# Kernel tuning notes

Hardware: AMD Instinct MI355X
Metric: run time of the kernel (lower is better)

Reference implementation:

```python
import jax, jax.numpy as jnp
import numpy as np
from jax import lax

BITS = 8

def dec2bin(q, bits=BITS):
    # q: integer-valued float tensor (NCHW or OIHW); stack two's-complement bit-planes along axis 1
    u = jnp.mod(jnp.round(q).astype(jnp.int32), 2 ** bits)
    return jnp.concatenate([((u >> k) & 1) for k in range(bits)], axis=1).astype(jnp.float32)

def quant_sym(x, bits=BITS):
    # brevitas-style signed symmetric per-tensor fake-quant (zero_point = 0)
    n = 2.0 ** (bits - 1) - 1.0
    scale = jnp.max(jnp.abs(x)) / n
    q = jnp.clip(jnp.round(x / scale), -n, n)  # q == value/scale + zero_point
    return q * scale, q

def quant_relu(x, bits=BITS):
    # QuantReLU: unsigned per-tensor fake-quant after relu
    r = jnp.maximum(x, 0.0)
    n = 2.0 ** bits - 1.0
    scale = jnp.max(r) / n
    q = jnp.clip(jnp.round(r / scale), 0.0, n)
    return q * scale, q

def conv(x, w, stride, pad):
    return lax.conv_general_dilated(x, w, (stride, stride), [(pad, pad), (pad, pad)],
                                    dimension_numbers=('NCHW', 'OIHW', 'NCHW'))

def bn(x, g, b, m, v, eps=1e-5):
    inv = g * lax.rsqrt(v + eps)
    return x * inv[None, :, None, None] + (b - m * inv)[None, :, None, None]

def setup_inputs() -> dict:
    key = jax.random.key(0)
    ks = jax.random.split(key, 11)
    N, C, H, W = 16, 64, 56, 56
    return {
        'x':  jax.random.normal(ks[0], (N, C, H, W), jnp.float32),
        'w1': jax.random.normal(ks[1], (C, C, 3, 3), jnp.float32) * 0.05,
        'w2': jax.random.normal(ks[2], (C, C, 3, 3), jnp.float32) * 0.05,
        'g1': jax.random.uniform(ks[3], (C,), jnp.float32, 0.5, 1.5),
        'b1': jax.random.normal(ks[4], (C,), jnp.float32) * 0.1,
        'm1': jax.random.normal(ks[5], (C,), jnp.float32) * 0.1,
        'v1': jax.random.uniform(ks[6], (C,), jnp.float32, 0.5, 1.5),
        'g2': jax.random.uniform(ks[7], (C,), jnp.float32, 0.5, 1.5),
        'b2': jax.random.normal(ks[8], (C,), jnp.float32) * 0.1,
        'm2': jax.random.normal(ks[9], (C,), jnp.float32) * 0.1,
        'v2': jax.random.uniform(ks[10], (C,), jnp.float32, 0.5, 1.5),
    }

def reference(x, w1, w2, g1, b1, m1, v1, g2, b2, m2, v2):
    stride = 1
    # quant_input (QuantIdentity) produces the quant tensor entering the block
    xq, qx = quant_sym(x)
    identity = xq
    # HM_activation: total number of set bits in the int activation
    HM_act = jnp.sum(dec2bin(qx))
    # HM_energy: L1 norm of conv over bit-decomposed int activations/weights
    w1q, qw1 = quant_sym(w1)
    HM_energy = jnp.sum(jnp.abs(conv(dec2bin(qx), dec2bin(qw1), stride, 1)))
    # conv1 -> bn1 -> QuantReLU
    o = bn(conv(xq, w1q, stride, 1), g1, b1, m1, v1)
    o1, q1 = quant_relu(o)
    HM_act = HM_act + jnp.sum(dec2bin(q1))
    w2q, qw2 = quant_sym(w2)
    HM_energy = HM_energy + jnp.sum(jnp.abs(conv(dec2bin(q1), dec2bin(qw2), 1, 1)))
    # conv2 -> bn2 -> residual add -> QuantReLU
    o = bn(conv(o1, w2q, 1, 1), g2, b2, m2, v2)
    o = o + identity
    out, _ = quant_relu(o)
    return out, HM_act, HM_energy
```

## Files before the change

kernel.cpp:

```cpp
#include <hip/hip_runtime.h>

using u32 = unsigned int;
typedef int v4i __attribute__((ext_vector_type(4)));

constexpr int N_IMG   = 16;
constexpr int PADROW  = 4096;
constexpr int ROWS_PI = 58;

constexpr size_t OFS_QX   = 4096;
constexpr size_t SZ_QPAD  = (size_t)(1 + N_IMG * ROWS_PI) * PADROW;
constexpr size_t OFS_Q1   = OFS_QX + SZ_QPAD;
constexpr size_t OFS_O1   = OFS_Q1 + SZ_QPAD;
constexpr size_t SZ_OF    = (size_t)N_IMG * 56 * 56 * 64 * 4;
constexpr size_t OFS_O2   = OFS_O1 + SZ_OF;
constexpr size_t OFS_QW1  = OFS_O2 + SZ_OF;
constexpr size_t OFS_QW2  = OFS_QW1 + 36864;
constexpr size_t OFS_WB1  = OFS_QW2 + 36864;
constexpr size_t OFS_WB2  = OFS_WB1 + 18432;
constexpr size_t OFS_WSUM = OFS_WB2 + 18432;
constexpr size_t OFS_SCAL = OFS_WSUM + 256;
constexpr size_t OFS_STX  = OFS_SCAL + 384;
constexpr size_t OFS_STQ  = OFS_STX + 18432;
constexpr size_t OFS_WSRED= OFS_STQ + 18432;
constexpr size_t WS_NEED  = OFS_WSRED + 4096;
constexpr size_t ZSPAN    = OFS_WSRED - OFS_WSUM;
constexpr size_t OUTN     = (size_t)16 * 64 * 56 * 56;

static __device__ __forceinline__ float block_redmax(float v, float* red, int t) {
    red[t] = v; __syncthreads();
    for (int s = 128; s > 0; s >>= 1) {
        if (t < s) red[t] = fmaxf(red[t], red[t + s]);
        __syncthreads();
    }
    float r = red[0]; __syncthreads();
    return r;
}

__global__ __launch_bounds__(256) void k_absmax_qw(const float* __restrict__ x,
                                                   const float* __restrict__ w1,
                                                   const float* __restrict__ w2,
                                                   char* __restrict__ qw1, char* __restrict__ qw2,
                                                   int* __restrict__ wb1, int* __restrict__ wb2,
                                                   int* __restrict__ wsum, float* __restrict__ scal,
                                                   float* __restrict__ wsred) {
    __shared__ union { float red[256]; int wsl[256]; } sm;
    int b = blockIdx.x, t = threadIdx.x;
    if (b >= 18) {
        int xb = b - 18;
        float mx = 0.f;
        const float4* p4 = (const float4*)x;
        for (int i = xb * 256 + t; i < 802816; i += 1024 * 256) {
            float4 v = p4[i];
            mx = fmaxf(mx, fmaxf(fmaxf(fabsf(v.x), fabsf(v.y)),
                                 fmaxf(fabsf(v.z), fabsf(v.w))));
        }
        mx = block_redmax(mx, sm.red, t);
        if (t == 0) wsred[xb] = mx;
        return;
    }
    int wsel = b / 9, kp = b - wsel * 9;
    const float* w = wsel ? w2 : w1;
    char* qw = wsel ? qw2 : qw1;
    int* wb  = wsel ? wb2 : wb1;
    float mx = 0.f;
    const float4* p4 = (const float4*)w;
    for (int i = t; i < 9216; i += 256) {
        float4 v = p4[i];
        mx = fmaxf(mx, fmaxf(fmaxf(fabsf(v.x), fabsf(v.y)),
                             fmaxf(fabsf(v.z), fabsf(v.w))));
    }
    float maxW = block_redmax(mx, sm.red, t);
    if (t == 0 && kp == 0) scal[1 + wsel] = maxW;
    float s = maxW / 127.f;
    int co = t & 63, cg = t >> 6, ci0 = cg * 16;
    signed char qv[16];
    int qsum = 0;
#pragma unroll
    for (int i = 0; i < 16; i++) {
        int ci = ci0 + i;
        float v = w[((size_t)co * 64 + ci) * 9 + kp];
        float qf = rintf(v / s);
        qf = fminf(fmaxf(qf, -127.f), 127.f);
        int q = (int)qf;
        qv[i] = (signed char)q;
        qsum += q;
    }
    u32 pk[4];
#pragma unroll
    for (int d = 0; d < 4; d++)
        pk[d] = ((u32)(unsigned char)qv[d*4]) | ((u32)(unsigned char)qv[d*4+1] << 8)
              | ((u32)(unsigned char)qv[d*4+2] << 16) | ((u32)(unsigned char)qv[d*4+3] << 24);
    *(uint4*)&qw[(size_t)(kp * 64 + co) * 64 + ci0] = *(uint4*)pk;
#pragma unroll
    for (int i = 0; i < 16; i++) {
        u32 uu = (u32)(unsigned char)qv[i];
#pragma unroll
        for (int k = 0; k < 8; k++) {
            unsigned long long bal = __ballot((uu >> k) & 1);
            if (co == 0) wb[((ci0 + i) * 8 + k) * 9 + kp] = __popcll(bal);
        }
    }
    if (wsel == 1) {
        __syncthreads();
        sm.wsl[t] = qsum; __syncthreads();
        if (t < 64)
            atomicAdd(&wsum[t], sm.wsl[t] + sm.wsl[t + 64] + sm.wsl[t + 128] + sm.wsl[t + 192]);
    }
}

__global__ __launch_bounds__(256) void k_quant_x(const float* __restrict__ x,
                                                 char* __restrict__ qpad,
                                                 const float* __restrict__ wsred,
                                                 float* __restrict__ scal) {
    __shared__ union { float red[256]; char lq[4096]; } sm;
    int n = blockIdx.x, yy = blockIdx.y, t = threadIdx.x;
    u32* row = (u32*)(qpad + (size_t)(1 + n * ROWS_PI + yy) * PADROW);
    if (n == 0 && yy == 0) {
        u32* r0 = (u32*)qpad;
        for (int j = t; j < 1024; j += 256) r0[j] = 0u;
    }
    if (yy == 0 || yy == 57) {
        for (int j = t; j < 1024; j += 256) row[j] = 0u;
        return;
    }
    float a = fmaxf(fmaxf(wsred[t], wsred[t + 256]),
                    fmaxf(wsred[t + 512], wsred[t + 768]));
    float maxX = block_redmax(a, sm.red, t);
    if (n == 0 && yy == 1 && t == 0) scal[0] = maxX;
    int y = yy - 1;
    float sxq = maxX / 127.f;
    const float4* xr = (const float4*)(x + (size_t)n * 200704 + (size_t)y * 56);
    for (int j = t; j < 896; j += 256) {
        int c = j / 14, xq = j - c * 14;
        float4 v = xr[(size_t)c * 784 + xq];
#pragma unroll
        for (int i = 0; i < 4; i++) {
            float q = rintf(((const float*)&v)[i] / sxq);
            q = fminf(fmaxf(q, -127.f), 127.f);
            sm.lq[(4 * xq + i) * 64 + c] = (char)(int)q;
        }
    }
    __syncthreads();
    u32* lqd = (u32*)sm.lq;
    for (int j = t; j < 1024; j += 256) row[j] = (j < 896) ? lqd[j] : 0u;
}

static __device__ __forceinline__ void unpack_acc(u32 v, u32 pk[8]) {
#pragma unroll
    for (int k = 0; k < 8; k++) pk[k] += (v >> k) & 0x01010101u;
}

static __device__ __forceinline__ void reduce_cat(u32* red, int* gdst, const u32 pk[8],
                                                  bool active, int t) {
#pragma unroll
    for (int k = 0; k < 8; k++) red[t * 9 + k] = active ? pk[k] : 0u;
    __syncthreads();
#pragma unroll
    for (int p = t; p < 512; p += 256) {
        int ci = p >> 3, k = p & 7, ci4 = ci >> 2, bb = ci & 3;
        int sum = 0;
#pragma unroll
        for (int xo = 0; xo < 16; xo++)
            sum += (red[(xo * 16 + ci4) * 9 + k] >> (8 * bb)) & 0xFF;
        if (sum) atomicAdd(&gdst[p], sum);
    }
    __syncthreads();
}

template <int FROMF>
static __device__ __forceinline__ u32 pk_at(const u32* img, const float* ofb, float s1,
                                            u32 xm, int row, int xx, int ci4) {
    if (FROMF) {
        float4 v = *(const float4*)(ofb + (size_t)row * 3584 + xx * 64 + ci4 * 4);
        u32 pk = 0;
#pragma unroll
        for (int i = 0; i < 4; i++) {
            float vv = fmaxf(((const float*)&v)[i], 0.f);
            u32 q = (u32)(int)fminf(rintf(vv / s1), 255.f);
            pk |= q << (8 * i);
        }
        return pk;
    }
    return img[(size_t)row * 1024 + xx * 16 + ci4] ^ xm;
}

template <int FROMF>
static __device__ void stats_unit(u32* red, const char* qpad, const float* of, float s1,
                                  u32 xorm, int* gst, int s, int t) {
    int n = s >> 3, slab = s & 7;
    int ci4 = t & 15, xo = t >> 4;
    const u32* img = FROMF ? nullptr : (const u32*)(qpad + (size_t)(2 + n * ROWS_PI) * PADROW);
    const float* ofb = FROMF ? (of + (size_t)n * 56 * 3584) : nullptr;
    u32 xm = xorm * 0x01010101u;
    int y0 = slab * 7;
    {
        u32 pk[8] = {0,0,0,0,0,0,0,0};
#pragma unroll
        for (int r = 0; r < 7; r++)
#pragma unroll
            for (int j = 0; j < 4; j++) {
                int xx = xo + 16 * j;
                if (xx < 56) unpack_acc(pk_at<FROMF>(img, ofb, s1, xm, y0 + r, xx, ci4), pk);
            }
        reduce_cat(red, gst + 0 * 512, pk, true, t);
    }
    {
        u32 pk[8] = {0,0,0,0,0,0,0,0};
        bool act = (xo == 0);
        if (act)
#pragma unroll
            for (int r = 0; r < 7; r++)
                unpack_acc(pk_at<FROMF>(img, ofb, s1, xm, y0 + r, 0, ci4), pk);
        reduce_cat(red, gst + 3 * 512, pk, act, t);
    }
    {
        u32 pk[8] = {0,0,0,0,0,0,0,0};
        bool act = (xo == 7);
        if (act)
#pragma unroll
            for (int r = 0; r < 7; r++)
                unpack_acc(pk_at<FROMF>(img, ofb, s1, xm, y0 + r, 55, ci4), pk);
        reduce_cat(red, gst + 4 * 512, pk, act, t);
    }
    if (slab == 0) {
        u32 pk[8] = {0,0,0,0,0,0,0,0};
#pragma unroll
        for (int j = 0; j < 4; j++) {
            int xx = xo + 16 * j;
            if (xx < 56) unpack_acc(pk_at<FROMF>(img, ofb, s1, xm, 0, xx, ci4), pk);
        }
        reduce_cat(red, gst + 1 * 512, pk, true, t);
        if (t < 32) {
            int which = t >> 4, c4 = t & 15;
            u32 v = pk_at<FROMF>(img, ofb, s1, xm, 0, which ? 55 : 0, c4);
            for (int b = 0; b < 4; b++)
                for (int k = 0; k < 8; k++)
                    if ((v >> (8 * b + k)) & 1)
                        atomicAdd(&gst[(5 + which) * 512 + (c4 * 4 + b) * 8 + k], 1);
        }
    }
    if (slab == 7) {
        u32 pk[8] = {0,0,0,0,0,0,0,0};
#pragma unroll
        for (int j = 0; j < 4; j++) {
            int xx = xo + 16 * j;
            if (xx < 56) unpack_acc(pk_at<FROMF>(img, ofb, s1, xm, 55, xx, ci4), pk);
        }
        reduce_cat(red, gst + 2 * 512, pk, true, t);
        if (t < 32) {
            int which = t >> 4, c4 = t & 15;
            u32 v = pk_at<FROMF>(img, ofb, s1, xm, 55, which ? 55 : 0, c4);
            for (int b = 0; b < 4; b++)
                for (int k = 0; k < 8; k++)
                    if ((v >> (8 * b + k)) & 1)
                        atomicAdd(&gst[(7 + which) * 512 + (c4 * 4 + b) * 8 + k], 1);
        }
    }
}

template <int SECOND>
__global__ __launch_bounds__(256, 2) void k_conv(const char* __restrict__ qin,
                                                 const char* __restrict__ qw,
                                                 const int* __restrict__ wsum,
                                                 const char* __restrict__ qid,
                                                 const float* __restrict__ gg, const float* __restrict__ bb,
                                                 const float* __restrict__ mmp, const float* __restrict__ vvp,
                                                 const float* __restrict__ scal,
                                                 float* __restrict__ outp, u32* __restrict__ rmaxp) {
    __shared__ float red[4];
    int b = blockIdx.x, t = threadIdx.x;
    int w = t >> 6, lane = t & 63, mq = lane & 15, quad = lane >> 4;
    int u0 = b * 2;
    int n = u0 / 56, y = u0 - n * 56;
    const v4i* qin4 = (const v4i*)qin;
    size_t rbase = (size_t)(1 + n * ROWS_PI + y) * 256;
    v4i acc[2][4] = {{{0,0,0,0},{0,0,0,0},{0,0,0,0},{0,0,0,0}},
                     {{0,0,0,0},{0,0,0,0},{0,0,0,0},{0,0,0,0}}};
#pragma unroll
    for (int tap = 0; tap < 9; tap++) {
        const int ky = tap / 3, kx = tap - ky * 3;
        v4i bf[4];
#pragma unroll
        for (int nt = 0; nt < 4; nt++)
            bf[nt] = *(const v4i*)&qw[(size_t)((tap * 64 + nt * 16 + mq) << 6) + quad * 16];
        int px = w * 16 + mq + kx;
#pragma unroll
        for (int rr = 0; rr < 2; rr++) {
            v4i a = qin4[rbase + (size_t)(rr + ky) * 256 - 4 + px * 4 + quad];
#pragma unroll
            for (int nt = 0; nt < 4; nt++)
                acc[rr][nt] = __builtin_amdgcn_mfma_i32_16x16x64_i8(a, bf[nt], acc[rr][nt], 0, 0, 0);
        }
    }
    float sIn = SECOND ? __uint_as_float(((const u32*)scal)[32]) / 255.f : scal[0] / 127.f;
    float sW  = scal[1 + SECOND] / 127.f;
    float sx  = scal[0] / 127.f;
    float alpha[4], beta[4]; int wofs[4];
#pragma unroll
    for (int nt = 0; nt < 4; nt++) {
        int co = nt * 16 + mq;
        float inv = gg[co] * rsqrtf(vvp[co] + 1e-5f);
        alpha[nt] = sIn * sW * inv;
        beta[nt]  = bb[co] - mmp[co] * inv;
        wofs[nt]  = SECOND ? (wsum[co] << 7) : 0;
    }
    float lmax = 0.f;
#pragma unroll
    for (int rr = 0; rr < 2; rr++) {
        int uu = u0 + rr, yr = y + rr;
        size_t rowb = (size_t)uu * 3584;
        const signed char* idrow = SECOND
            ? (const signed char*)(qid + (size_t)(2 + n * ROWS_PI + yr) * PADROW) : nullptr;
#pragma unroll
        for (int nt = 0; nt < 4; nt++) {
            int co = nt * 16 + mq;
#pragma unroll
            for (int r = 0; r < 4; r++) {
                int xx = w * 16 + quad * 4 + r;
                if (xx < 56) {
                    float o = (float)(acc[rr][nt][r] + wofs[nt]) * alpha[nt] + beta[nt];
                    if (SECOND) o += sx * (float)idrow[xx * 64 + co];
                    outp[rowb + xx * 64 + co] = o;
                    lmax = fmaxf(lmax, o);
                }
            }
        }
    }
#pragma unroll
    for (int off = 32; off > 0; off >>= 1) lmax = fmaxf(lmax, __shfl_down(lmax, off));
    if (lane == 0) red[w] = lmax;
    __syncthreads();
    if (t == 0)
        atomicMax(rmaxp, __float_as_uint(fmaxf(fmaxf(red[0], red[1]), fmaxf(red[2], red[3]))));
}

__global__ __launch_bounds__(256) void k_qrelu1(const float* __restrict__ o1,
                                                char* __restrict__ q1,
                                                const char* __restrict__ qx,
                                                const float* __restrict__ scal,
                                                int* __restrict__ stx, int* __restrict__ stq) {
    __shared__ u32 sred[2304];
    int b = blockIdx.x, t = threadIdx.x;
    if (b >= 1056) {
        float s1 = __uint_as_float(((const u32*)scal)[32]) / 255.f;
        stats_unit<1>(sred, nullptr, o1, s1, 0u, stq, b - 1056, t);
        return;
    }
    if (b >= 928) { stats_unit<0>(sred, qx, nullptr, 0.f, 0u, stx, b - 928, t); return; }
    int n = b / 58, yy = b - n * 58;
    u32* row = (u32*)(q1 + (size_t)(1 + n * ROWS_PI + yy) * PADROW);
    if (n == 0 && yy == 0) {
        u32* r0 = (u32*)q1;
        for (int j = t; j < 1024; j += 256) r0[j] = 0x80808080u;
    }
    if (yy == 0 || yy == 57) {
        for (int j = t; j < 1024; j += 256) row[j] = 0x80808080u;
        return;
    }
    int y = yy - 1;
    float s1 = __uint_as_float(((const u32*)scal)[32]) / 255.f;
    const float4* o4 = (const float4*)(o1 + (size_t)(n * 56 + y) * 3584);
    for (int j = t; j < 1024; j += 256) {
        u32 pk = 0x80808080u;
        if (j < 896) {
            float4 v = o4[j];
            pk = 0u;
#pragma unroll
            for (int i = 0; i < 4; i++) {
                float vv = fmaxf(((const float*)&v)[i], 0.f);
                float q = fminf(rintf(vv / s1), 255.f);
                pk |= ((u32)(unsigned char)(char)((int)q - 128)) << (8 * i);
            }
        }
        row[j] = pk;
    }
}

__global__ __launch_bounds__(256) void k_final(const float* __restrict__ o2,
                                               const float* __restrict__ scal,
                                               float* __restrict__ outp,
                                               const int* __restrict__ stx, const int* __restrict__ stq,
                                               const int* __restrict__ wb1, const int* __restrict__ wb2) {
    __shared__ union { float lt[64 * 57]; long long r1[256]; } sm;
    int b = blockIdx.x, t = threadIdx.x;
    if (b == 448) {
        long long act = 0, en = 0;
#pragma unroll
        for (int half = 0; half < 2; half++) {
            int tt = t + half * 256;
#pragma unroll
            for (int wsel = 0; wsel < 2; wsel++) {
                const int* st = wsel ? stq : stx;
                const int* wb = wsel ? wb2 : wb1;
                long long s[9];
#pragma unroll
                for (int j = 0; j < 9; j++) s[j] = st[j * 512 + tt];
                int wr[9];
#pragma unroll
                for (int j = 0; j < 9; j++) wr[j] = wb[tt * 9 + j];
                long long wall = 0;
#pragma unroll
                for (int j = 0; j < 9; j++) wall += wr[j];
                long long wr0 = (long long)wr[0] + wr[1] + wr[2];
                long long wr2 = (long long)wr[6] + wr[7] + wr[8];
                long long wc0 = (long long)wr[0] + wr[3] + wr[6];
                long long wc2 = (long long)wr[2] + wr[5] + wr[8];
                en += s[0] * wall - s[1] * wr2 - s[2] * wr0 - s[3] * wc2 - s[4] * wc0
                    + s[5] * (long long)wr[8] + s[6] * (long long)wr[6]
                    + s[7] * (long long)wr[2] + s[8] * (long long)wr[0];
                act += s[0];
            }
        }
        sm.r1[t] = en; __syncthreads();
        for (int s = 128; s > 0; s >>= 1) { if (t < s) sm.r1[t] += sm.r1[t + s]; __syncthreads(); }
        long long etot = sm.r1[0]; __syncthreads();
        sm.r1[t] = act; __syncthreads();
        for (int s = 128; s > 0; s >>= 1) { if (t < s) sm.r1[t] += sm.r1[t + s]; __syncthreads(); }
        if (t == 0) {
            outp[OUTN]     = (float)sm.r1[0];
            outp[OUTN + 1] = (float)etot;
        }
        return;
    }
    float s2 = __uint_as_float(((const u32*)scal)[64]) / 255.f;
#pragma unroll
    for (int rr = 0; rr < 2; rr++) {
        int u = b * 2 + rr;
        int n = u / 56, y = u - n * 56;
        __syncthreads();
        const float4* o4 = (const float4*)(o2 + (size_t)u * 3584);
        for (int j = t; j < 896; j += 256) {
            int xx = j >> 4, c4 = j & 15;
            float4 v = o4[j];
#pragma unroll
            for (int i = 0; i < 4; i++) {
                float vv = fmaxf(((const float*)&v)[i], 0.f);
                float q = fminf(rintf(vv / s2), 255.f);
                sm.lt[(4 * c4 + i) * 57 + xx] = q * s2;
            }
        }
        __syncthreads();
        for (int idx = t; idx < 3584; idx += 256) {
            int co = idx / 56, xx = idx - co * 56;
            outp[(size_t)n * 200704 + (size_t)co * 3136 + y * 56 + xx] = sm.lt[co * 57 + xx];
        }
    }
}

extern "C" void kernel_launch(void* const* d_in, const int* in_sizes, int n_in,
                              void* d_out, int out_size, void* d_ws, size_t ws_size,
                              hipStream_t stream) {
    if (ws_size < WS_NEED) return;
    const float* x  = (const float*)d_in[0];
    const float* w1 = (const float*)d_in[1];
    const float* w2 = (const float*)d_in[2];
    const float* g1 = (const float*)d_in[3];
    const float* b1 = (const float*)d_in[4];
    const float* m1 = (const float*)d_in[5];
    const float* v1 = (const float*)d_in[6];
    const float* g2 = (const float*)d_in[7];
    const float* b2 = (const float*)d_in[8];
    const float* m2 = (const float*)d_in[9];
    const float* v2 = (const float*)d_in[10];
    char* ws = (char*)d_ws;
    char* qx  = ws + OFS_QX;
    char* q1  = ws + OFS_Q1;
    float* o1 = (float*)(ws + OFS_O1);
    float* o2 = (float*)(ws + OFS_O2);
    char* qw1 = ws + OFS_QW1;
    char* qw2 = ws + OFS_QW2;
    int* wb1  = (int*)(ws + OFS_WB1);
    int* wb2  = (int*)(ws + OFS_WB2);
    int* wsum = (int*)(ws + OFS_WSUM);
    float* scal = (float*)(ws + OFS_SCAL);
    u32* rmax1 = (u32*)(ws + OFS_SCAL + 128);
    u32* rmax2 = (u32*)(ws + OFS_SCAL + 256);
    int* stx  = (int*)(ws + OFS_STX);
    int* stq  = (int*)(ws + OFS_STQ);
    float* wsred = (float*)(ws + OFS_WSRED);
    float* outp = (float*)d_out;

    (void)hipMemsetAsync(ws + OFS_WSUM, 0, ZSPAN, stream);
    k_absmax_qw<<<1042, 256, 0, stream>>>(x, w1, w2, qw1, qw2, wb1, wb2, wsum, scal, wsred);
    k_quant_x<<<dim3(16, 58), 256, 0, stream>>>(x, qx, wsred, scal);
    k_conv<0><<<448, 256, 0, stream>>>(qx, qw1, wsum, nullptr,
                                       g1, b1, m1, v1, scal, o1, rmax1);
    k_qrelu1<<<1184, 256, 0, stream>>>(o1, q1, qx, scal, stx, stq);
    k_conv<1><<<448, 256, 0, stream>>>(q1, qw2, wsum, qx,
                                       g2, b2, m2, v2, scal, o2, rmax2);
    k_final<<<449, 256, 0, stream>>>(o2, scal, outp, stx, stq, wb1, wb2);
}
```

Measured before the change: 176.1 us.

## Move bit-stat reductions into conv kernels and drop memset launch

The bit-plane statistics blocks now run as extra blocks inside the two conv launches instead of inside the qrelu kernel. The q1 statistics are read from the already-quantized padded byte buffer, with an XOR of 0x80 to correct its pad encoding, rather than re-quantizing o1 from floats. The hipMemsetAsync is replaced by zeroing inside the first kernel. The weight-sum atomics become per-tap plain stores, and conv2 sums those nine partials itself. This removes one launch and redundant float reads, and lets the stats work overlap with conv, at the cost of more blocks sharing the conv grid and a larger shared-memory union in conv.

```diff
diff --git a/kernel.cpp b/kernel.cpp
--- a/kernel.cpp
+++ b/kernel.cpp
@@ -18,12 +18,11 @@
 constexpr size_t OFS_WB1  = OFS_QW2 + 36864;
 constexpr size_t OFS_WB2  = OFS_WB1 + 18432;
 constexpr size_t OFS_WSUM = OFS_WB2 + 18432;
-constexpr size_t OFS_SCAL = OFS_WSUM + 256;
+constexpr size_t OFS_SCAL = OFS_WSUM + 2304;
 constexpr size_t OFS_STX  = OFS_SCAL + 384;
 constexpr size_t OFS_STQ  = OFS_STX + 18432;
 constexpr size_t OFS_WSRED= OFS_STQ + 18432;
 constexpr size_t WS_NEED  = OFS_WSRED + 4096;
-constexpr size_t ZSPAN    = OFS_WSRED - OFS_WSUM;
 constexpr size_t OUTN     = (size_t)16 * 64 * 56 * 56;
 
 static __device__ __forceinline__ float block_redmax(float v, float* red, int t) {
@@ -41,12 +40,16 @@
                                                    const float* __restrict__ w2,
                                                    char* __restrict__ qw1, char* __restrict__ qw2,
                                                    int* __restrict__ wb1, int* __restrict__ wb2,
-                                                   int* __restrict__ wsum, float* __restrict__ scal,
-                                                   float* __restrict__ wsred) {
+                                                   int* __restrict__ wsum9, float* __restrict__ scal,
+                                                   float* __restrict__ wsred,
+                                                   int* __restrict__ stx, int* __restrict__ stq) {
     __shared__ union { float red[256]; int wsl[256]; } sm;
     int b = blockIdx.x, t = threadIdx.x;
     if (b >= 18) {
         int xb = b - 18;
+        if (b == 18) for (int i = t; i < 4608; i += 256) stx[i] = 0;
+        if (b == 19) for (int i = t; i < 4608; i += 256) stq[i] = 0;
+        if (b == 20 && t == 0) { ((u32*)scal)[32] = 0u; ((u32*)scal)[64] = 0u; }
         float mx = 0.f;
         const float4* p4 = (const float4*)x;
         for (int i = xb * 256 + t; i < 802816; i += 1024 * 256) {
@@ -104,7 +107,7 @@
         __syncthreads();
         sm.wsl[t] = qsum; __syncthreads();
         if (t < 64)
-            atomicAdd(&wsum[t], sm.wsl[t] + sm.wsl[t + 64] + sm.wsl[t + 128] + sm.wsl[t + 192]);
+            wsum9[kp * 64 + t] = sm.wsl[t] + sm.wsl[t + 64] + sm.wsl[t + 128] + sm.wsl[t + 192];
     }
 }
 
@@ -167,41 +170,23 @@
     __syncthreads();
 }
 
-template <int FROMF>
-static __device__ __forceinline__ u32 pk_at(const u32* img, const float* ofb, float s1,
-                                            u32 xm, int row, int xx, int ci4) {
-    if (FROMF) {
-        float4 v = *(const float4*)(ofb + (size_t)row * 3584 + xx * 64 + ci4 * 4);
-        u32 pk = 0;
-#pragma unroll
-        for (int i = 0; i < 4; i++) {
-            float vv = fmaxf(((const float*)&v)[i], 0.f);
-            u32 q = (u32)(int)fminf(rintf(vv / s1), 255.f);
-            pk |= q << (8 * i);
-        }
-        return pk;
-    }
-    return img[(size_t)row * 1024 + xx * 16 + ci4] ^ xm;
-}
-
-template <int FROMF>
-static __device__ void stats_unit(u32* red, const char* qpad, const float* of, float s1,
-                                  u32 xorm, int* gst, int s, int t) {
+static __device__ void stats_unit(u32* red, const char* qpad, u32 xorm, int* gst, int s, int t) {
     int n = s >> 3, slab = s & 7;
     int ci4 = t & 15, xo = t >> 4;
-    const u32* img = FROMF ? nullptr : (const u32*)(qpad + (size_t)(2 + n * ROWS_PI) * PADROW);
-    const float* ofb = FROMF ? (of + (size_t)n * 56 * 3584) : nullptr;
+    const u32* img = (const u32*)(qpad + (size_t)(2 + n * ROWS_PI) * PADROW);
     u32 xm = xorm * 0x01010101u;
     int y0 = slab * 7;
     {
         u32 pk[8] = {0,0,0,0,0,0,0,0};
 #pragma unroll
-        for (int r = 0; r < 7; r++)
+        for (int r = 0; r < 7; r++) {
+            const u32* row = img + (size_t)(y0 + r) * 1024;
 #pragma unroll
             for (int j = 0; j < 4; j++) {
                 int xx = xo + 16 * j;
-                if (xx < 56) unpack_acc(pk_at<FROMF>(img, ofb, s1, xm, y0 + r, xx, ci4), pk);
+                if (xx < 56) unpack_acc(row[xx * 16 + ci4] ^ xm, pk);
             }
+        }
         reduce_cat(red, gst + 0 * 512, pk, true, t);
     }
     {
@@ -210,7 +195,7 @@
         if (act)
 #pragma unroll
             for (int r = 0; r < 7; r++)
-                unpack_acc(pk_at<FROMF>(img, ofb, s1, xm, y0 + r, 0, ci4), pk);
+                unpack_acc(img[(size_t)(y0 + r) * 1024 + ci4] ^ xm, pk);
         reduce_cat(red, gst + 3 * 512, pk, act, t);
     }
     {
@@ -219,7 +204,7 @@
         if (act)
 #pragma unroll
             for (int r = 0; r < 7; r++)
-                unpack_acc(pk_at<FROMF>(img, ofb, s1, xm, y0 + r, 55, ci4), pk);
+                unpack_acc(img[(size_t)(y0 + r) * 1024 + 55 * 16 + ci4] ^ xm, pk);
         reduce_cat(red, gst + 4 * 512, pk, act, t);
     }
     if (slab == 0) {
@@ -227,12 +212,12 @@
 #pragma unroll
         for (int j = 0; j < 4; j++) {
             int xx = xo + 16 * j;
-            if (xx < 56) unpack_acc(pk_at<FROMF>(img, ofb, s1, xm, 0, xx, ci4), pk);
+            if (xx < 56) unpack_acc(img[xx * 16 + ci4] ^ xm, pk);
         }
         reduce_cat(red, gst + 1 * 512, pk, true, t);
         if (t < 32) {
             int which = t >> 4, c4 = t & 15;
-            u32 v = pk_at<FROMF>(img, ofb, s1, xm, 0, which ? 55 : 0, c4);
+            u32 v = img[(which ? 55 : 0) * 16 + c4] ^ xm;
             for (int b = 0; b < 4; b++)
                 for (int k = 0; k < 8; k++)
                     if ((v >> (8 * b + k)) & 1)
@@ -244,12 +229,12 @@
 #pragma unroll
         for (int j = 0; j < 4; j++) {
             int xx = xo + 16 * j;
-            if (xx < 56) unpack_acc(pk_at<FROMF>(img, ofb, s1, xm, 55, xx, ci4), pk);
+            if (xx < 56) unpack_acc(img[(size_t)55 * 1024 + xx * 16 + ci4] ^ xm, pk);
         }
         reduce_cat(red, gst + 2 * 512, pk, true, t);
         if (t < 32) {
             int which = t >> 4, c4 = t & 15;
-            u32 v = pk_at<FROMF>(img, ofb, s1, xm, 55, which ? 55 : 0, c4);
+            u32 v = img[(size_t)55 * 1024 + (which ? 55 : 0) * 16 + c4] ^ xm;
             for (int b = 0; b < 4; b++)
                 for (int k = 0; k < 8; k++)
                     if ((v >> (8 * b + k)) & 1)
@@ -261,14 +246,19 @@
 template <int SECOND>
 __global__ __launch_bounds__(256, 2) void k_conv(const char* __restrict__ qin,
                                                  const char* __restrict__ qw,
-                                                 const int* __restrict__ wsum,
+                                                 const int* __restrict__ wsum9,
                                                  const char* __restrict__ qid,
                                                  const float* __restrict__ gg, const float* __restrict__ bb,
                                                  const float* __restrict__ mmp, const float* __restrict__ vvp,
                                                  const float* __restrict__ scal,
-                                                 float* __restrict__ outp, u32* __restrict__ rmaxp) {
-    __shared__ float red[4];
+                                                 float* __restrict__ outp, u32* __restrict__ rmaxp,
+                                                 int* __restrict__ gst) {
+    __shared__ union { float red[4]; u32 sred[2304]; } sm;
     int b = blockIdx.x, t = threadIdx.x;
+    if (b >= 448) {
+        stats_unit(sm.sred, qin, SECOND ? 0x80u : 0u, gst, b - 448, t);
+        return;
+    }
     int w = t >> 6, lane = t & 63, mq = lane & 15, quad = lane >> 4;
     int u0 = b * 2;
     int n = u0 / 56, y = u0 - n * 56;
@@ -302,7 +292,12 @@
         float inv = gg[co] * rsqrtf(vvp[co] + 1e-5f);
         alpha[nt] = sIn * sW * inv;
         beta[nt]  = bb[co] - mmp[co] * inv;
-        wofs[nt]  = SECOND ? (wsum[co] << 7) : 0;
+        int ws9 = 0;
+        if (SECOND) {
+#pragma unroll
+            for (int kp = 0; kp < 9; kp++) ws9 += wsum9[kp * 64 + co];
+        }
+        wofs[nt] = SECOND ? (ws9 << 7) : 0;
     }
     float lmax = 0.f;
 #pragma unroll
@@ -328,25 +323,17 @@
     }
 #pragma unroll
     for (int off = 32; off > 0; off >>= 1) lmax = fmaxf(lmax, __shfl_down(lmax, off));
-    if (lane == 0) red[w] = lmax;
+    if (lane == 0) sm.red[w] = lmax;
     __syncthreads();
     if (t == 0)
-        atomicMax(rmaxp, __float_as_uint(fmaxf(fmaxf(red[0], red[1]), fmaxf(red[2], red[3]))));
+        atomicMax(rmaxp, __float_as_uint(fmaxf(fmaxf(sm.red[0], sm.red[1]),
+                                               fmaxf(sm.red[2], sm.red[3]))));
 }
 
 __global__ __launch_bounds__(256) void k_qrelu1(const float* __restrict__ o1,
                                                 char* __restrict__ q1,
-                                                const char* __restrict__ qx,
-                                                const float* __restrict__ scal,
-                                                int* __restrict__ stx, int* __restrict__ stq) {
-    __shared__ u32 sred[2304];
+                                                const float* __restrict__ scal) {
     int b = blockIdx.x, t = threadIdx.x;
-    if (b >= 1056) {
-        float s1 = __uint_as_float(((const u32*)scal)[32]) / 255.f;
-        stats_unit<1>(sred, nullptr, o1, s1, 0u, stq, b - 1056, t);
-        return;
-    }
-    if (b >= 928) { stats_unit<0>(sred, qx, nullptr, 0.f, 0u, stx, b - 928, t); return; }
     int n = b / 58, yy = b - n * 58;
     u32* row = (u32*)(q1 + (size_t)(1 + n * ROWS_PI + yy) * PADROW);
     if (n == 0 && yy == 0) {
@@ -471,7 +458,7 @@
     char* qw2 = ws + OFS_QW2;
     int* wb1  = (int*)(ws + OFS_WB1);
     int* wb2  = (int*)(ws + OFS_WB2);
-    int* wsum = (int*)(ws + OFS_WSUM);
+    int* wsum9= (int*)(ws + OFS_WSUM);
     float* scal = (float*)(ws + OFS_SCAL);
     u32* rmax1 = (u32*)(ws + OFS_SCAL + 128);
     u32* rmax2 = (u32*)(ws + OFS_SCAL + 256);
@@ -480,13 +467,13 @@
     float* wsred = (float*)(ws + OFS_WSRED);
     float* outp = (float*)d_out;
 
-    (void)hipMemsetAsync(ws + OFS_WSUM, 0, ZSPAN, stream);
-    k_absmax_qw<<<1042, 256, 0, stream>>>(x, w1, w2, qw1, qw2, wb1, wb2, wsum, scal, wsred);
+    k_absmax_qw<<<1042, 256, 0, stream>>>(x, w1, w2, qw1, qw2, wb1, wb2,
+                                          wsum9, scal, wsred, stx, stq);
     k_quant_x<<<dim3(16, 58), 256, 0, stream>>>(x, qx, wsred, scal);
-    k_conv<0><<<448, 256, 0, stream>>>(qx, qw1, wsum, nullptr,
-                                       g1, b1, m1, v1, scal, o1, rmax1);
-    k_qrelu1<<<1184, 256, 0, stream>>>(o1, q1, qx, scal, stx, stq);
-    k_conv<1><<<448, 256, 0, stream>>>(q1, qw2, wsum, qx,
-                                       g2, b2, m2, v2, scal, o2, rmax2);
+    k_conv<0><<<576, 256, 0, stream>>>(qx, qw1, wsum9, nullptr,
+                                       g1, b1, m1, v1, scal, o1, rmax1, stx);
+    k_qrelu1<<<928, 256, 0, stream>>>(o1, q1, scal);
+    k_conv<1><<<576, 256, 0, stream>>>(q1, qw2, wsum9, qx,
+                                       g2, b2, m2, v2, scal, o2, rmax2, stq);
     k_final<<<449, 256, 0, stream>>>(o2, scal, outp, stx, stq, wb1, wb2);
 }
```

After: 169.0 us. 1.04x faster.

## Fuse ReLU requantization into conv2 via LDS staging and drop memset

Applied to the files above, without the earlier changes.

Removes the separate quant-relu kernel that wrote the padded int8 q1 tensor. Conv2 now reads the fp32 conv1 output, quantizes three input rows into LDS itself, and runs the MFMA loop from shared memory. The statistics blocks move into the two conv launches as extra blocks. The weight-sum atomics become per-tap plain stores, and the zeroing is done inside the first kernel, so the memset launch disappears. In exchange, conv2 re-reads and re-quantizes overlapping halo rows from fp32 (about three times the reads of a byte tensor), and its larger LDS footprint may reduce occupancy.

```diff
diff --git a/kernel.cpp b/kernel.cpp
--- a/kernel.cpp
+++ b/kernel.cpp
@@ -18,12 +18,11 @@
 constexpr size_t OFS_WB1  = OFS_QW2 + 36864;
 constexpr size_t OFS_WB2  = OFS_WB1 + 18432;
 constexpr size_t OFS_WSUM = OFS_WB2 + 18432;
-constexpr size_t OFS_SCAL = OFS_WSUM + 256;
+constexpr size_t OFS_SCAL = OFS_WSUM + 2304;
 constexpr size_t OFS_STX  = OFS_SCAL + 384;
 constexpr size_t OFS_STQ  = OFS_STX + 18432;
 constexpr size_t OFS_WSRED= OFS_STQ + 18432;
 constexpr size_t WS_NEED  = OFS_WSRED + 4096;
-constexpr size_t ZSPAN    = OFS_WSRED - OFS_WSUM;
 constexpr size_t OUTN     = (size_t)16 * 64 * 56 * 56;
 
 static __device__ __forceinline__ float block_redmax(float v, float* red, int t) {
@@ -41,12 +40,16 @@
                                                    const float* __restrict__ w2,
                                                    char* __restrict__ qw1, char* __restrict__ qw2,
                                                    int* __restrict__ wb1, int* __restrict__ wb2,
-                                                   int* __restrict__ wsum, float* __restrict__ scal,
-                                                   float* __restrict__ wsred) {
+                                                   int* __restrict__ wsum9, float* __restrict__ scal,
+                                                   float* __restrict__ wsred,
+                                                   int* __restrict__ stx, int* __restrict__ stq) {
     __shared__ union { float red[256]; int wsl[256]; } sm;
     int b = blockIdx.x, t = threadIdx.x;
     if (b >= 18) {
         int xb = b - 18;
+        if (b == 18) for (int i = t; i < 4608; i += 256) stx[i] = 0;
+        if (b == 19) for (int i = t; i < 4608; i += 256) stq[i] = 0;
+        if (b == 20 && t == 0) { ((u32*)scal)[32] = 0u; ((u32*)scal)[64] = 0u; }
         float mx = 0.f;
         const float4* p4 = (const float4*)x;
         for (int i = xb * 256 + t; i < 802816; i += 1024 * 256) {
@@ -104,7 +107,7 @@
         __syncthreads();
         sm.wsl[t] = qsum; __syncthreads();
         if (t < 64)
-            atomicAdd(&wsum[t], sm.wsl[t] + sm.wsl[t + 64] + sm.wsl[t + 128] + sm.wsl[t + 192]);
+            wsum9[kp * 64 + t] = sm.wsl[t] + sm.wsl[t + 64] + sm.wsl[t + 128] + sm.wsl[t + 192];
     }
 }
 
@@ -258,17 +261,19 @@
     }
 }
 
-template <int SECOND>
-__global__ __launch_bounds__(256, 2) void k_conv(const char* __restrict__ qin,
-                                                 const char* __restrict__ qw,
-                                                 const int* __restrict__ wsum,
-                                                 const char* __restrict__ qid,
-                                                 const float* __restrict__ gg, const float* __restrict__ bb,
-                                                 const float* __restrict__ mmp, const float* __restrict__ vvp,
-                                                 const float* __restrict__ scal,
-                                                 float* __restrict__ outp, u32* __restrict__ rmaxp) {
-    __shared__ float red[4];
+__global__ __launch_bounds__(256, 2) void k_conv1(const char* __restrict__ qin,
+                                                  const char* __restrict__ qw,
+                                                  const float* __restrict__ gg, const float* __restrict__ bb,
+                                                  const float* __restrict__ mmp, const float* __restrict__ vvp,
+                                                  const float* __restrict__ scal,
+                                                  float* __restrict__ outp, u32* __restrict__ rmaxp,
+                                                  int* __restrict__ gst) {
+    __shared__ union { float red[4]; u32 sred[2304]; } sm;
     int b = blockIdx.x, t = threadIdx.x;
+    if (b >= 448) {
+        stats_unit<0>(sm.sred, qin, nullptr, 0.f, 0u, gst, b - 448, t);
+        return;
+    }
     int w = t >> 6, lane = t & 63, mq = lane & 15, quad = lane >> 4;
     int u0 = b * 2;
     int n = u0 / 56, y = u0 - n * 56;
@@ -292,25 +297,20 @@
                 acc[rr][nt] = __builtin_amdgcn_mfma_i32_16x16x64_i8(a, bf[nt], acc[rr][nt], 0, 0, 0);
         }
     }
-    float sIn = SECOND ? __uint_as_float(((const u32*)scal)[32]) / 255.f : scal[0] / 127.f;
-    float sW  = scal[1 + SECOND] / 127.f;
-    float sx  = scal[0] / 127.f;
-    float alpha[4], beta[4]; int wofs[4];
+    float sIn = scal[0] / 127.f;
+    float sW  = scal[1] / 127.f;
+    float alpha[4], beta[4];
 #pragma unroll
     for (int nt = 0; nt < 4; nt++) {
         int co = nt * 16 + mq;
         float inv = gg[co] * rsqrtf(vvp[co] + 1e-5f);
         alpha[nt] = sIn * sW * inv;
         beta[nt]  = bb[co] - mmp[co] * inv;
-        wofs[nt]  = SECOND ? (wsum[co] << 7) : 0;
     }
     float lmax = 0.f;
 #pragma unroll
     for (int rr = 0; rr < 2; rr++) {
-        int uu = u0 + rr, yr = y + rr;
-        size_t rowb = (size_t)uu * 3584;
-        const signed char* idrow = SECOND
-            ? (const signed char*)(qid + (size_t)(2 + n * ROWS_PI + yr) * PADROW) : nullptr;
+        size_t rowb = (size_t)(u0 + rr) * 3584;
 #pragma unroll
         for (int nt = 0; nt < 4; nt++) {
             int co = nt * 16 + mq;
@@ -318,8 +318,7 @@
             for (int r = 0; r < 4; r++) {
                 int xx = w * 16 + quad * 4 + r;
                 if (xx < 56) {
-                    float o = (float)(acc[rr][nt][r] + wofs[nt]) * alpha[nt] + beta[nt];
-                    if (SECOND) o += sx * (float)idrow[xx * 64 + co];
+                    float o = (float)acc[rr][nt][r] * alpha[nt] + beta[nt];
                     outp[rowb + xx * 64 + co] = o;
                     lmax = fmaxf(lmax, o);
                 }
@@ -328,52 +327,115 @@
     }
 #pragma unroll
     for (int off = 32; off > 0; off >>= 1) lmax = fmaxf(lmax, __shfl_down(lmax, off));
-    if (lane == 0) red[w] = lmax;
+    if (lane == 0) sm.red[w] = lmax;
     __syncthreads();
     if (t == 0)
-        atomicMax(rmaxp, __float_as_uint(fmaxf(fmaxf(red[0], red[1]), fmaxf(red[2], red[3]))));
-}
-
-__global__ __launch_bounds__(256) void k_qrelu1(const float* __restrict__ o1,
-                                                char* __restrict__ q1,
-                                                const char* __restrict__ qx,
-                                                const float* __restrict__ scal,
-                                                int* __restrict__ stx, int* __restrict__ stq) {
-    __shared__ u32 sred[2304];
+        atomicMax(rmaxp, __float_as_uint(fmaxf(fmaxf(sm.red[0], sm.red[1]),
+                                               fmaxf(sm.red[2], sm.red[3]))));
+}
+
+__global__ __launch_bounds__(256, 2) void k_conv2f(const float* __restrict__ o1,
+                                                   const char* __restrict__ qw,
+                                                   const int* __restrict__ wsum9,
+                                                   const char* __restrict__ qid,
+                                                   const float* __restrict__ gg, const float* __restrict__ bb,
+                                                   const float* __restrict__ mmp, const float* __restrict__ vvp,
+                                                   const float* __restrict__ scal,
+                                                   float* __restrict__ outp, u32* __restrict__ rmaxp,
+                                                   int* __restrict__ gst) {
+    __shared__ union { struct { u32 lin[5280]; float red[4]; } c; u32 sred[2304]; } sm;
     int b = blockIdx.x, t = threadIdx.x;
-    if (b >= 1056) {
-        float s1 = __uint_as_float(((const u32*)scal)[32]) / 255.f;
-        stats_unit<1>(sred, nullptr, o1, s1, 0u, stq, b - 1056, t);
+    float s1 = __uint_as_float(((const u32*)scal)[32]) / 255.f;
+    if (b >= 448) {
+        stats_unit<1>(sm.sred, nullptr, o1, s1, 0u, gst, b - 448, t);
         return;
     }
-    if (b >= 928) { stats_unit<0>(sred, qx, nullptr, 0.f, 0u, stx, b - 928, t); return; }
-    int n = b / 58, yy = b - n * 58;
-    u32* row = (u32*)(q1 + (size_t)(1 + n * ROWS_PI + yy) * PADROW);
-    if (n == 0 && yy == 0) {
-        u32* r0 = (u32*)q1;
-        for (int j = t; j < 1024; j += 256) r0[j] = 0x80808080u;
-    }
-    if (yy == 0 || yy == 57) {
-        for (int j = t; j < 1024; j += 256) row[j] = 0x80808080u;
-        return;
-    }
-    int y = yy - 1;
-    float s1 = __uint_as_float(((const u32*)scal)[32]) / 255.f;
-    const float4* o4 = (const float4*)(o1 + (size_t)(n * 56 + y) * 3584);
-    for (int j = t; j < 1024; j += 256) {
-        u32 pk = 0x80808080u;
-        if (j < 896) {
-            float4 v = o4[j];
-            pk = 0u;
+    int w = t >> 6, lane = t & 63, mq = lane & 15, quad = lane >> 4;
+    int u0 = b * 2;
+    int n = u0 / 56, y = u0 - n * 56;
+    for (int j = t; j < 5280; j += 256) sm.c.lin[j] = 0x80808080u;
+    __syncthreads();
+    for (int j = t; j < 3584; j += 256) {
+        int lr = j >> 10;
+        lr = j / 896;
+        int r = j - lr * 896;
+        int ry = y - 1 + lr;
+        if (ry >= 0 && ry <= 55) {
+            int px = r >> 4, cd = r & 15;
+            float4 v = *(const float4*)(o1 + (size_t)(n * 56 + ry) * 3584 + (px << 6) + (cd << 2));
+            u32 pk = 0;
 #pragma unroll
             for (int i = 0; i < 4; i++) {
                 float vv = fmaxf(((const float*)&v)[i], 0.f);
                 float q = fminf(rintf(vv / s1), 255.f);
                 pk |= ((u32)(unsigned char)(char)((int)q - 128)) << (8 * i);
             }
-        }
-        row[j] = pk;
-    }
+            sm.c.lin[(lr * 66 + px + 1) * 20 + cd] = pk;
+        }
+    }
+    __syncthreads();
+    v4i acc[2][4] = {{{0,0,0,0},{0,0,0,0},{0,0,0,0},{0,0,0,0}},
+                     {{0,0,0,0},{0,0,0,0},{0,0,0,0},{0,0,0,0}}};
+#pragma unroll
+    for (int tap = 0; tap < 9; tap++) {
+        const int ky = tap / 3, kx = tap - ky * 3;
+        v4i bf[4];
+#pragma unroll
+        for (int nt = 0; nt < 4; nt++)
+            bf[nt] = *(const v4i*)&qw[(size_t)((tap * 64 + nt * 16 + mq) << 6) + quad * 16];
+        int px = w * 16 + mq + kx;
+#pragma unroll
+        for (int rr = 0; rr < 2; rr++) {
+            v4i a = *(const v4i*)&sm.c.lin[((rr + ky) * 66 + px) * 20 + quad * 4];
+#pragma unroll
+            for (int nt = 0; nt < 4; nt++)
+                acc[rr][nt] = __builtin_amdgcn_mfma_i32_16x16x64_i8(a, bf[nt], acc[rr][nt], 0, 0, 0);
+        }
+    }
+    float sIn = s1;
+    float sW  = scal[2] / 127.f;
+    float sx  = scal[0] / 127.f;
+    float alpha[4], beta[4]; int wofs[4];
+#pragma unroll
+    for (int nt = 0; nt < 4; nt++) {
+        int co = nt * 16 + mq;
+        float inv = gg[co] * rsqrtf(vvp[co] + 1e-5f);
+        alpha[nt] = sIn * sW * inv;
+        beta[nt]  = bb[co] - mmp[co] * inv;
+        int ws9 = 0;
+#pragma unroll
+        for (int kp = 0; kp < 9; kp++) ws9 += wsum9[kp * 64 + co];
+        wofs[nt] = ws9 << 7;
+    }
+    float lmax = 0.f;
+#pragma unroll
+    for (int rr = 0; rr < 2; rr++) {
+        int yr = y + rr;
+        size_t rowb = (size_t)(u0 + rr) * 3584;
+        const signed char* idrow =
+            (const signed char*)(qid + (size_t)(2 + n * ROWS_PI + yr) * PADROW);
+#pragma unroll
+        for (int nt = 0; nt < 4; nt++) {
+            int co = nt * 16 + mq;
+#pragma unroll
+            for (int r = 0; r < 4; r++) {
+                int xx = w * 16 + quad * 4 + r;
+                if (xx < 56) {
+                    float o = (float)(acc[rr][nt][r] + wofs[nt]) * alpha[nt] + beta[nt];
+                    o += sx * (float)idrow[xx * 64 + co];
+                    outp[rowb + xx * 64 + co] = o;
+                    lmax = fmaxf(lmax, o);
+                }
+            }
+        }
+    }
+#pragma unroll
+    for (int off = 32; off > 0; off >>= 1) lmax = fmaxf(lmax, __shfl_down(lmax, off));
+    if (lane == 0) sm.c.red[w] = lmax;
+    __syncthreads();
+    if (t == 0)
+        atomicMax(rmaxp, __float_as_uint(fmaxf(fmaxf(sm.c.red[0], sm.c.red[1]),
+                                               fmaxf(sm.c.red[2], sm.c.red[3]))));
 }
 
 __global__ __launch_bounds__(256) void k_final(const float* __restrict__ o2,
@@ -464,14 +526,13 @@
     const float* v2 = (const float*)d_in[10];
     char* ws = (char*)d_ws;
     char* qx  = ws + OFS_QX;
-    char* q1  = ws + OFS_Q1;
     float* o1 = (float*)(ws + OFS_O1);
     float* o2 = (float*)(ws + OFS_O2);
     char* qw1 = ws + OFS_QW1;
     char* qw2 = ws + OFS_QW2;
     int* wb1  = (int*)(ws + OFS_WB1);
     int* wb2  = (int*)(ws + OFS_WB2);
-    int* wsum = (int*)(ws + OFS_WSUM);
+    int* wsum9= (int*)(ws + OFS_WSUM);
     float* scal = (float*)(ws + OFS_SCAL);
     u32* rmax1 = (u32*)(ws + OFS_SCAL + 128);
     u32* rmax2 = (u32*)(ws + OFS_SCAL + 256);
@@ -480,13 +541,11 @@
     float* wsred = (float*)(ws + OFS_WSRED);
     float* outp = (float*)d_out;
 
-    (void)hipMemsetAsync(ws + OFS_WSUM, 0, ZSPAN, stream);
-    k_absmax_qw<<<1042, 256, 0, stream>>>(x, w1, w2, qw1, qw2, wb1, wb2, wsum, scal, wsred);
+    k_absmax_qw<<<1042, 256, 0, stream>>>(x, w1, w2, qw1, qw2, wb1, wb2,
+                                          wsum9, scal, wsred, stx, stq);
     k_quant_x<<<dim3(16, 58), 256, 0, stream>>>(x, qx, wsred, scal);
-    k_conv<0><<<448, 256, 0, stream>>>(qx, qw1, wsum, nullptr,
-                                       g1, b1, m1, v1, scal, o1, rmax1);
-    k_qrelu1<<<1184, 256, 0, stream>>>(o1, q1, qx, scal, stx, stq);
-    k_conv<1><<<448, 256, 0, stream>>>(q1, qw2, wsum, qx,
-                                       g2, b2, m2, v2, scal, o2, rmax2);
+    k_conv1<<<576, 256, 0, stream>>>(qx, qw1, g1, b1, m1, v1, scal, o1, rmax1, stx);
+    k_conv2f<<<576, 256, 0, stream>>>(o1, qw2, wsum9, qx, g2, b2, m2, v2,
+                                      scal, o2, rmax2, stq);
     k_final<<<449, 256, 0, stream>>>(o2, scal, outp, stx, stq, wb1, wb2);
 }
```

After: 166.8 us. -5.3%, faster.
